# Optimization experiments

Hardware: AMD Instinct MI355X
Metric: run time of the kernel (lower is better)

The kernel has to match this reference:

```python
import jax, jax.numpy as jnp
import numpy as np

N_NODES = 50000   # nodes per channel
N_EDGES = 800000  # intra edges per channel (avg degree ~16)
N_GRAPHS = 64     # graphs in the batch (global_add_pool segments)
D = 128           # node_features_len == out_channels
L = 3             # n_layers
BN_EPS = 1e-5
NEG_SLOPE = 0.01  # F.leaky_relu default


def setup_inputs() -> dict:
    key = jax.random.key(0)
    ks = jax.random.split(key, 24)
    s = 0.05
    inp = {
        "x1": jax.random.normal(ks[0], (N_NODES, D), jnp.float32),
        "x2": jax.random.normal(ks[1], (N_NODES, D), jnp.float32),
        # GIN MLP channel 1: Linear-BN-ReLU-Linear-ReLU, stacked over layers
        "W1_ch1": jax.random.normal(ks[2], (L, D, D), jnp.float32) * s,
        "b1_ch1": jax.random.normal(ks[3], (L, D), jnp.float32) * s,
        "bn_g": 1.0 + jax.random.normal(ks[4], (L, D), jnp.float32) * s,
        "bn_b": jax.random.normal(ks[5], (L, D), jnp.float32) * s,
        "bn_m": jax.random.normal(ks[6], (L, D), jnp.float32) * s,
        "bn_v": 0.5 + jax.random.uniform(ks[7], (L, D), jnp.float32),
        "W2_ch1": jax.random.normal(ks[8], (L, D, D), jnp.float32) * s,
        "b2_ch1": jax.random.normal(ks[9], (L, D), jnp.float32) * s,
        # GIN MLP channel 2: Linear-ReLU-Linear
        "W1_ch2": jax.random.normal(ks[10], (L, D, D), jnp.float32) * s,
        "b1_ch2": jax.random.normal(ks[11], (L, D), jnp.float32) * s,
        "W2_ch2": jax.random.normal(ks[12], (L, D, D), jnp.float32) * s,
        "b2_ch2": jax.random.normal(ks[13], (L, D), jnp.float32) * s,
        # head: Linear(2*D*L -> D) - ReLU - Dropout - Linear(D -> 1)
        "Wf1": jax.random.normal(ks[14], (2 * D * L, D), jnp.float32) * s,
        "bf1": jax.random.normal(ks[15], (D,), jnp.float32) * s,
        "Wf2": jax.random.normal(ks[16], (D, 1), jnp.float32) * s,
        "bf2": jax.random.normal(ks[17], (1,), jnp.float32) * s,
        "edge1": jax.random.randint(ks[18], (2, N_EDGES), 0, N_NODES, dtype=jnp.int32),
        "edge2": jax.random.randint(ks[19], (2, N_EDGES), 0, N_NODES, dtype=jnp.int32),
        "batch1": jnp.sort(jax.random.randint(ks[20], (N_NODES,), 0, N_GRAPHS, dtype=jnp.int32)),
        "batch2": jnp.sort(jax.random.randint(ks[21], (N_NODES,), 0, N_GRAPHS, dtype=jnp.int32)),
    }
    return inp


def _aggregate(x, edge):
    # GINConv sum aggregation: message x[src] scattered to dst; eps=0 default
    return jax.ops.segment_sum(x[edge[0]], edge[1], num_segments=N_NODES)


def _channel1(x, edge, batch, W1, b1, g, b, m, v, W2, b2):
    pooled = []
    for i in range(L):
        h = (x + _aggregate(x, edge)) @ W1[i] + b1[i]
        h = (h - m[i]) * (g[i] / jnp.sqrt(v[i] + BN_EPS)) + b[i]  # eval-mode BN
        h = jax.nn.relu(h)
        h = jax.nn.relu(h @ W2[i] + b2[i])
        x = jax.nn.leaky_relu(h, NEG_SLOPE)
        pooled.append(jax.ops.segment_sum(x, batch, num_segments=N_GRAPHS))
    return jnp.concatenate(pooled, axis=-1)  # [G, D*L]


def _channel2(x, edge, batch, W1, b1, W2, b2):
    pooled = []
    for i in range(L):
        h = jax.nn.relu((x + _aggregate(x, edge)) @ W1[i] + b1[i])
        h = h @ W2[i] + b2[i]
        x = jax.nn.leaky_relu(h, NEG_SLOPE)
        pooled.append(jax.ops.segment_sum(x, batch, num_segments=N_GRAPHS))
    return jnp.concatenate(pooled, axis=-1)  # [G, D*L]


def reference(x1, x2, W1_ch1, b1_ch1, bn_g, bn_b, bn_m, bn_v, W2_ch1, b2_ch1,
              W1_ch2, b1_ch2, W2_ch2, b2_ch2, Wf1, bf1, Wf2, bf2,
              edge1, edge2, batch1, batch2):
    p1 = _channel1(x1, edge1, batch1, W1_ch1, b1_ch1, bn_g, bn_b, bn_m, bn_v, W2_ch1, b2_ch1)
    p2 = _channel2(x2, edge2, batch2, W1_ch2, b1_ch2, W2_ch2, b2_ch2)
    z = jnp.concatenate([p1, p2], axis=-1)  # [G, 2*D*L]
    h = jax.nn.relu(z @ Wf1 + bf1)          # dropout is identity in eval mode
    return h @ Wf2 + bf2                    # [G, 1]
```

## Files before the change

kernel.cpp:

```cpp
#include <hip/hip_runtime.h>

#define NN 50000
#define NE 800000
#define TOTN (2 * NN)
#define NG 64
#define DD 128
#define NL 3
#define ZW (2 * DD * NL)
#define NB2 128
#define NPB 391
#define CAP2 8192
#define CHUNK 4096
#define P1B 196
#define GB2 1024
#define AGGB (TOTN / 16)
#define CVTX (TOTN * DD / 8 / 256)

typedef __attribute__((ext_vector_type(8))) short short8;
typedef __attribute__((ext_vector_type(4))) float f32x4;

__device__ inline unsigned short f2bf(float f) {
  unsigned int u = __float_as_uint(f);
  unsigned int r = (u + 0x7fffu + ((u >> 16) & 1u)) >> 16;
  return (unsigned short)r;
}
__device__ inline float bflo(unsigned int u) { return __uint_as_float(u << 16); }
__device__ inline float bfhi(unsigned int u) { return __uint_as_float(u & 0xffff0000u); }

__global__ __launch_bounds__(256) void prep_kernel(
    const float* __restrict__ x1, const float* __restrict__ x2,
    unsigned short* __restrict__ X,
    const float* __restrict__ p0, const float* __restrict__ p1,
    const float* __restrict__ p2, const float* __restrict__ p3,
    unsigned short* __restrict__ WT,
    const int* __restrict__ e1, const int* __restrict__ e2,
    int* __restrict__ bcur, uint2* __restrict__ pairs) {
  int bid = blockIdx.x;
  if (bid < CVTX) {
    int i = bid * 256 + threadIdx.x;
    const int per = NN * DD / 8;
    int ch = i >= per;
    const float* x = ch ? x2 : x1;
    int il = i - ch * per;
    const float4* in4 = reinterpret_cast<const float4*>(x);
    float4 a = in4[2 * il], b = in4[2 * il + 1];
    uint4 o;
    o.x = (unsigned int)f2bf(a.x) | ((unsigned int)f2bf(a.y) << 16);
    o.y = (unsigned int)f2bf(a.z) | ((unsigned int)f2bf(a.w) << 16);
    o.z = (unsigned int)f2bf(b.x) | ((unsigned int)f2bf(b.y) << 16);
    o.w = (unsigned int)f2bf(b.z) | ((unsigned int)f2bf(b.w) << 16);
    reinterpret_cast<uint4*>(X)[i] = o;
    return;
  }
  if (bid < CVTX + 192) {
    __shared__ float tile[32][33];
    int idx = bid - CVTX;
    int k0 = (idx & 3) * 32, c0 = ((idx >> 2) & 3) * 32, slot = idx >> 4;
    int grp = slot / 3, mat = slot % 3;
    const float* ip = (grp == 0 ? p0 : grp == 1 ? p1 : grp == 2 ? p2 : p3) + mat * 16384;
    unsigned short* op = WT + slot * 16384;
    int tx = threadIdx.x & 31, ty = threadIdx.x >> 5;
#pragma unroll
    for (int rr = 0; rr < 32; rr += 8)
      tile[ty + rr][tx] = ip[(k0 + ty + rr) * 128 + (c0 + tx)];
    __syncthreads();
#pragma unroll
    for (int rr = 0; rr < 32; rr += 8)
      op[(c0 + ty + rr) * 128 + (k0 + tx)] = f2bf(tile[tx][ty + rr]);
    return;
  }
  {
    int blk = bid - (CVTX + 192);
    int ch = blk >= P1B;
    blk -= ch * P1B;
    const int* E = ch ? e2 : e1;
    int base = blk * CHUNK;
    __shared__ int lcnt[NB2], gbase[NB2];
    for (int i = threadIdx.x; i < NB2; i += 256) lcnt[i] = 0;
    __syncthreads();
    int srcv[16], dstv[16], lrank[16];
#pragma unroll
    for (int k = 0; k < 16; k++) {
      int e = base + k * 256 + threadIdx.x;
      if (e < NE) {
        srcv[k] = E[e];
        dstv[k] = E[NE + e];
        lrank[k] = atomicAdd(&lcnt[dstv[k] / NPB], 1);
      } else dstv[k] = -1;
    }
    __syncthreads();
    for (int i = threadIdx.x; i < NB2; i += 256)
      gbase[i] = atomicAdd(&bcur[ch * NB2 + i], lcnt[i]);
    __syncthreads();
#pragma unroll
    for (int k = 0; k < 16; k++)
      if (dstv[k] >= 0) {
        int g = dstv[k] / NPB;
        pairs[(size_t)(ch * NB2 + g) * CAP2 + gbase[g] + lrank[k]] =
            make_uint2((unsigned)srcv[k], (unsigned)dstv[k]);
      }
  }
}

__global__ __launch_bounds__(256) void scan_gstart_kernel(const int* __restrict__ bcur,
                                                          int* __restrict__ colbase,
                                                          const int* __restrict__ batch1,
                                                          const int* __restrict__ batch2,
                                                          int* __restrict__ gstart) {
  if (blockIdx.x == 0) {
    __shared__ int s[256];
    int tid = threadIdx.x;
    int v = bcur[tid];
    s[tid] = v;
    __syncthreads();
    int segstart = tid & ~127;
    for (int o = 1; o < 128; o <<= 1) {
      int t = (tid - o >= segstart) ? s[tid - o] : 0;
      __syncthreads();
      s[tid] += t;
      __syncthreads();
    }
    colbase[tid] = s[tid] - v;
  } else {
    int t = threadIdx.x;
    if (t >= 2 * (NG + 1)) return;
    int ch = t / (NG + 1), g = t % (NG + 1);
    const int* b = ch ? batch2 : batch1;
    int lo = 0, hi = NN;
    while (lo < hi) {
      int m = (lo + hi) >> 1;
      if (b[m] < g) lo = m + 1; else hi = m;
    }
    gstart[t] = lo;
  }
}

__global__ __launch_bounds__(256) void csr_build_kernel(const uint2* __restrict__ pairs,
                                                        const int* __restrict__ bcur,
                                                        const int* __restrict__ colbase,
                                                        int* __restrict__ rowptr,
                                                        int* __restrict__ col) {
  int g = blockIdx.x;
  int ch = g >> 7, b = g & 127;
  int node0 = b * NPB;
  int nloc = min(NPB, NN - node0);
  int count = bcur[g];
  int base = colbase[g];
  const uint2* p = pairs + (size_t)g * CAP2;
  __shared__ int hist[512], pref[512], cur[512], stmp[256];
  for (int i = threadIdx.x; i < 512; i += 256) hist[i] = 0;
  __syncthreads();
  for (int e = threadIdx.x; e < count; e += 256)
    atomicAdd(&hist[(int)p[e].y - node0], 1);
  __syncthreads();
  int t = threadIdx.x;
  int a0 = hist[2 * t], a1 = hist[2 * t + 1];
  int sum = a0 + a1;
  stmp[t] = sum;
  __syncthreads();
  for (int o = 1; o < 256; o <<= 1) {
    int tv = (t >= o) ? stmp[t - o] : 0;
    __syncthreads();
    stmp[t] += tv;
    __syncthreads();
  }
  int ex = stmp[t] - sum;
  pref[2 * t] = ex;       pref[2 * t + 1] = ex + a0;
  cur[2 * t] = ex;        cur[2 * t + 1] = ex + a0;
  __syncthreads();
  for (int i = threadIdx.x; i < nloc; i += 256)
    rowptr[ch * (NN + 1) + node0 + i] = base + pref[i];
  if (threadIdx.x == 0 && b == NB2 - 1) rowptr[ch * (NN + 1) + NN] = base + count;
  for (int e = threadIdx.x; e < count; e += 256) {
    uint2 pr = p[e];
    int pos = atomicAdd(&cur[(int)pr.y - node0], 1);
    col[ch * NE + base + pos] = (int)pr.x;
  }
}

__global__ __launch_bounds__(256) void agg_pool_kernel(const unsigned short* __restrict__ X,
                                                       const int* __restrict__ rowptr,
                                                       const int* __restrict__ col,
                                                       unsigned short* __restrict__ Y,
                                                       const unsigned short* __restrict__ Xprev,
                                                       const int* __restrict__ gstart,
                                                       float* __restrict__ z, int layerPrev) {
  if (blockIdx.x >= AGGB) {
    int pb = blockIdx.x - AGGB;
    int ch = pb >> 6, g = pb & 63;
    int r0 = gstart[ch * (NG + 1) + g], r1 = gstart[ch * (NG + 1) + g + 1];
    int c8 = threadIdx.x & 15, part = threadIdx.x >> 4;
    const uint4* X4 = reinterpret_cast<const uint4*>(Xprev);
    size_t base = (size_t)ch * NN * 16 + c8;
    float acc[8];
#pragma unroll
    for (int q = 0; q < 8; q++) acc[q] = 0.f;
    int r = r0 + part;
    for (; r + 48 < r1; r += 64) {
      uint4 v0 = X4[base + (size_t)r * 16];
      uint4 v1 = X4[base + (size_t)(r + 16) * 16];
      uint4 v2 = X4[base + (size_t)(r + 32) * 16];
      uint4 v3 = X4[base + (size_t)(r + 48) * 16];
      unsigned int w0[4] = {v0.x, v0.y, v0.z, v0.w};
      unsigned int w1[4] = {v1.x, v1.y, v1.z, v1.w};
      unsigned int w2[4] = {v2.x, v2.y, v2.z, v2.w};
      unsigned int w3[4] = {v3.x, v3.y, v3.z, v3.w};
#pragma unroll
      for (int q = 0; q < 4; q++) {
        acc[2 * q]     += bflo(w0[q]) + bflo(w1[q]) + bflo(w2[q]) + bflo(w3[q]);
        acc[2 * q + 1] += bfhi(w0[q]) + bfhi(w1[q]) + bfhi(w2[q]) + bfhi(w3[q]);
      }
    }
    for (; r < r1; r += 16) {
      uint4 v = X4[base + (size_t)r * 16];
      unsigned int w[4] = {v.x, v.y, v.z, v.w};
#pragma unroll
      for (int q = 0; q < 4; q++) {
        acc[2 * q]     += bflo(w[q]);
        acc[2 * q + 1] += bfhi(w[q]);
      }
    }
    __shared__ float zacc[16][128];
#pragma unroll
    for (int q = 0; q < 8; q++) zacc[part][c8 * 8 + q] = acc[q];
    __syncthreads();
    for (int s = 8; s > 0; s >>= 1) {
      if (part < s) {
#pragma unroll
        for (int q = 0; q < 8; q++)
          zacc[part][c8 * 8 + q] += zacc[part + s][c8 * 8 + q];
      }
      __syncthreads();
    }
    if (part == 0) {
#pragma unroll
      for (int q = 0; q < 8; q++) {
        int colw = c8 * 8 + q;
        z[(size_t)g * ZW + ch * DD * NL + layerPrev * DD + colw] = zacc[0][colw];
      }
    }
    return;
  }
  int node = blockIdx.x * 16 + (threadIdx.x >> 4);
  int lane = threadIdx.x & 15;
  int ch = node >= NN;
  int nl = node - ch * NN;
  const int* rp = rowptr + ch * (NN + 1);
  const int* cl = col + ch * NE;
  const uint4* X4 = reinterpret_cast<const uint4*>(X);
  size_t chbase = (size_t)ch * NN * 16;
  float acc[8];
  {
    uint4 sv = X4[(size_t)node * 16 + lane];
    unsigned int w[4] = {sv.x, sv.y, sv.z, sv.w};
#pragma unroll
    for (int q = 0; q < 4; q++) {
      acc[2 * q]     = bflo(w[q]);
      acc[2 * q + 1] = bfhi(w[q]);
    }
  }
  int s = rp[nl], e = rp[nl + 1];
  int j = s;
  for (; j + 8 <= e; j += 8) {
    uint4 v[8];
#pragma unroll
    for (int q = 0; q < 8; q++)
      v[q] = X4[chbase + (size_t)cl[j + q] * 16 + lane];
#pragma unroll
    for (int q = 0; q < 8; q++) {
      unsigned int w[4] = {v[q].x, v[q].y, v[q].z, v[q].w};
#pragma unroll
      for (int u = 0; u < 4; u++) {
        acc[2 * u]     += bflo(w[u]);
        acc[2 * u + 1] += bfhi(w[u]);
      }
    }
  }
  for (; j < e; ++j) {
    uint4 v = X4[chbase + (size_t)cl[j] * 16 + lane];
    unsigned int w[4] = {v.x, v.y, v.z, v.w};
#pragma unroll
    for (int u = 0; u < 4; u++) {
      acc[2 * u]     += bflo(w[u]);
      acc[2 * u + 1] += bfhi(w[u]);
    }
  }
  uint4 o;
  unsigned int* ow = reinterpret_cast<unsigned int*>(&o);
#pragma unroll
  for (int q = 0; q < 4; q++)
    ow[q] = (unsigned int)f2bf(acc[2 * q]) | ((unsigned int)f2bf(acc[2 * q + 1]) << 16);
  reinterpret_cast<uint4*>(Y)[(size_t)node * 16 + lane] = o;
}

__global__ __launch_bounds__(256) void gemm_fused_kernel(
    const unsigned short* __restrict__ Y, unsigned short* __restrict__ X,
    const unsigned short* __restrict__ WT,
    const float* __restrict__ b1c1, const float* __restrict__ b1c2,
    const float* __restrict__ b2c1, const float* __restrict__ b2c2,
    const float* __restrict__ bng, const float* __restrict__ bnb,
    const float* __restrict__ bnm, const float* __restrict__ bnv, int layer) {
  __shared__ unsigned short hlds[16][136];
  int ch = blockIdx.x >= GB2;
  int lane = threadIdx.x & 63, wv = threadIdx.x >> 6;
  int l15 = lane & 15, lk = lane >> 4;
  int c0 = wv * 32;
  const unsigned short* W1 = WT + (size_t)(ch * 6 + layer) * 16384;
  const unsigned short* W2 = WT + (size_t)(ch * 6 + 3 + layer) * 16384;
  short8 w1f[2][4], w2f[2][4];
#pragma unroll
  for (int ct = 0; ct < 2; ct++)
#pragma unroll
    for (int kk = 0; kk < 4; kk++) {
      size_t boff = (size_t)(c0 + ct * 16 + l15) * 128 + kk * 32 + lk * 8;
      w1f[ct][kk] = *reinterpret_cast<const short8*>(W1 + boff);
      w2f[ct][kk] = *reinterpret_cast<const short8*>(W2 + boff);
    }
  const float* b1 = (ch ? b1c2 : b1c1) + layer * DD;
  const float* b2 = (ch ? b2c2 : b2c1) + layer * DD;
  float sc1[2], sh1[2], sh2[2];
#pragma unroll
  for (int ct = 0; ct < 2; ct++) {
    int colg = c0 + ct * 16 + l15;
    if (!ch) {
      float s = bng[layer * DD + colg] * rsqrtf(bnv[layer * DD + colg] + 1e-5f);
      sc1[ct] = s;
      sh1[ct] = (b1[colg] - bnm[layer * DD + colg]) * s + bnb[layer * DD + colg];
    } else {
      sc1[ct] = 1.f;
      sh1[ct] = b1[colg];
    }
    sh2[ct] = b2[colg];
  }
  int t0 = ch ? blockIdx.x - GB2 : blockIdx.x;
  short8 a0, a1, a2, a3;
  {
    size_t r0g = (size_t)ch * NN + t0 * 16;
    const unsigned short* yp = Y + (r0g + l15) * 128 + lk * 8;
    a0 = *reinterpret_cast<const short8*>(yp);
    a1 = *reinterpret_cast<const short8*>(yp + 32);
    a2 = *reinterpret_cast<const short8*>(yp + 64);
    a3 = *reinterpret_cast<const short8*>(yp + 96);
  }
  for (int t = t0; t < 3125; t += GB2) {
    int r0l = t * 16;
    size_t r0g = (size_t)ch * NN + r0l;
    short8 n0, n1, n2, n3;
    int tn = t + GB2;
    if (tn < 3125) {
      const unsigned short* yp = Y + ((size_t)ch * NN + tn * 16 + l15) * 128 + lk * 8;
      n0 = *reinterpret_cast<const short8*>(yp);
      n1 = *reinterpret_cast<const short8*>(yp + 32);
      n2 = *reinterpret_cast<const short8*>(yp + 64);
      n3 = *reinterpret_cast<const short8*>(yp + 96);
    }
#pragma unroll
    for (int ct = 0; ct < 2; ct++) {
      f32x4 acc = {0.f, 0.f, 0.f, 0.f};
      acc = __builtin_amdgcn_mfma_f32_16x16x32_bf16(a0, w1f[ct][0], acc, 0, 0, 0);
      acc = __builtin_amdgcn_mfma_f32_16x16x32_bf16(a1, w1f[ct][1], acc, 0, 0, 0);
      acc = __builtin_amdgcn_mfma_f32_16x16x32_bf16(a2, w1f[ct][2], acc, 0, 0, 0);
      acc = __builtin_amdgcn_mfma_f32_16x16x32_bf16(a3, w1f[ct][3], acc, 0, 0, 0);
      int colg = c0 + ct * 16 + l15;
#pragma unroll
      for (int r = 0; r < 4; r++) {
        float tv = fmaxf(acc[r] * sc1[ct] + sh1[ct], 0.f);
        hlds[lk * 4 + r][colg] = f2bf(tv);
      }
    }
    __syncthreads();
    short8 h0 = *reinterpret_cast<const short8*>(&hlds[l15][lk * 8]);
    short8 h1 = *reinterpret_cast<const short8*>(&hlds[l15][32 + lk * 8]);
    short8 h2 = *reinterpret_cast<const short8*>(&hlds[l15][64 + lk * 8]);
    short8 h3 = *reinterpret_cast<const short8*>(&hlds[l15][96 + lk * 8]);
#pragma unroll
    for (int ct = 0; ct < 2; ct++) {
      f32x4 acc = {0.f, 0.f, 0.f, 0.f};
      acc = __builtin_amdgcn_mfma_f32_16x16x32_bf16(h0, w2f[ct][0], acc, 0, 0, 0);
      acc = __builtin_amdgcn_mfma_f32_16x16x32_bf16(h1, w2f[ct][1], acc, 0, 0, 0);
      acc = __builtin_amdgcn_mfma_f32_16x16x32_bf16(h2, w2f[ct][2], acc, 0, 0, 0);
      acc = __builtin_amdgcn_mfma_f32_16x16x32_bf16(h3, w2f[ct][3], acc, 0, 0, 0);
      int colg = c0 + ct * 16 + l15;
#pragma unroll
      for (int r = 0; r < 4; r++) {
        float tv = acc[r] + sh2[ct];
        if (!ch) tv = fmaxf(tv, 0.f);
        else     tv = tv > 0.f ? tv : 0.01f * tv;
        X[(r0g + lk * 4 + r) * 128 + colg] = f2bf(tv);
      }
    }
    __syncthreads();
    a0 = n0; a1 = n1; a2 = n2; a3 = n3;
  }
}

__global__ __launch_bounds__(256) void pool_kernel(const unsigned short* __restrict__ X,
                                                   const int* __restrict__ gstart,
                                                   float* __restrict__ z, int layer) {
  int ch = blockIdx.x >> 6, g = blockIdx.x & 63;
  int r0 = gstart[ch * (NG + 1) + g], r1 = gstart[ch * (NG + 1) + g + 1];
  int c8 = threadIdx.x & 15, part = threadIdx.x >> 4;
  const uint4* X4 = reinterpret_cast<const uint4*>(X);
  size_t base = (size_t)ch * NN * 16 + c8;
  float acc[8];
#pragma unroll
  for (int q = 0; q < 8; q++) acc[q] = 0.f;
  int r = r0 + part;
  for (; r + 48 < r1; r += 64) {
    uint4 v0 = X4[base + (size_t)r * 16];
    uint4 v1 = X4[base + (size_t)(r + 16) * 16];
    uint4 v2 = X4[base + (size_t)(r + 32) * 16];
    uint4 v3 = X4[base + (size_t)(r + 48) * 16];
    unsigned int w0[4] = {v0.x, v0.y, v0.z, v0.w};
    unsigned int w1[4] = {v1.x, v1.y, v1.z, v1.w};
    unsigned int w2[4] = {v2.x, v2.y, v2.z, v2.w};
    unsigned int w3[4] = {v3.x, v3.y, v3.z, v3.w};
#pragma unroll
    for (int q = 0; q < 4; q++) {
      acc[2 * q]     += bflo(w0[q]) + bflo(w1[q]) + bflo(w2[q]) + bflo(w3[q]);
      acc[2 * q + 1] += bfhi(w0[q]) + bfhi(w1[q]) + bfhi(w2[q]) + bfhi(w3[q]);
    }
  }
  for (; r < r1; r += 16) {
    uint4 v = X4[base + (size_t)r * 16];
    unsigned int w[4] = {v.x, v.y, v.z, v.w};
#pragma unroll
    for (int q = 0; q < 4; q++) {
      acc[2 * q]     += bflo(w[q]);
      acc[2 * q + 1] += bfhi(w[q]);
    }
  }
  __shared__ float zacc[16][128];
#pragma unroll
  for (int q = 0; q < 8; q++) zacc[part][c8 * 8 + q] = acc[q];
  __syncthreads();
  for (int s = 8; s > 0; s >>= 1) {
    if (part < s) {
#pragma unroll
      for (int q = 0; q < 8; q++)
        zacc[part][c8 * 8 + q] += zacc[part + s][c8 * 8 + q];
    }
    __syncthreads();
  }
  if (part == 0) {
#pragma unroll
    for (int q = 0; q < 8; q++) {
      int colw = c8 * 8 + q;
      z[(size_t)g * ZW + ch * DD * NL + layer * DD + colw] = zacc[0][colw];
    }
  }
}

__global__ __launch_bounds__(128) void head_kernel(const float* __restrict__ z,
                                                   const float* __restrict__ Wf1,
                                                   const float* __restrict__ bf1,
                                                   const float* __restrict__ Wf2,
                                                   const float* __restrict__ bf2,
                                                   float* __restrict__ out) {
  int g = blockIdx.x, t = threadIdx.x;
  const float* zr = z + (size_t)g * ZW;
  float acc = bf1[t];
  for (int j = 0; j < ZW; ++j) acc += zr[j] * Wf1[(size_t)j * DD + t];
  float h = fmaxf(acc, 0.f);
  __shared__ float red[128];
  red[t] = h * Wf2[t];
  __syncthreads();
  for (int s = 64; s > 0; s >>= 1) {
    if (t < s) red[t] += red[t + s];
    __syncthreads();
  }
  if (t == 0) out[g] = red[0] + bf2[0];
}

extern "C" void kernel_launch(void* const* d_in, const int* in_sizes, int n_in,
                              void* d_out, int out_size, void* d_ws, size_t ws_size,
                              hipStream_t stream) {
  const float* x1   = (const float*)d_in[0];
  const float* x2   = (const float*)d_in[1];
  const float* W1c1 = (const float*)d_in[2];
  const float* b1c1 = (const float*)d_in[3];
  const float* bng  = (const float*)d_in[4];
  const float* bnb  = (const float*)d_in[5];
  const float* bnm  = (const float*)d_in[6];
  const float* bnv  = (const float*)d_in[7];
  const float* W2c1 = (const float*)d_in[8];
  const float* b2c1 = (const float*)d_in[9];
  const float* W1c2 = (const float*)d_in[10];
  const float* b1c2 = (const float*)d_in[11];
  const float* W2c2 = (const float*)d_in[12];
  const float* b2c2 = (const float*)d_in[13];
  const float* Wf1  = (const float*)d_in[14];
  const float* bf1  = (const float*)d_in[15];
  const float* Wf2  = (const float*)d_in[16];
  const float* bf2  = (const float*)d_in[17];
  const int* edge1  = (const int*)d_in[18];
  const int* edge2  = (const int*)d_in[19];
  const int* batch1 = (const int*)d_in[20];
  const int* batch2 = (const int*)d_in[21];
  (void)ws_size; (void)n_in; (void)in_sizes; (void)out_size;

  char* ws = (char*)d_ws;
  const size_t NB16 = (size_t)TOTN * DD * 2;
  unsigned short* bufA = (unsigned short*)(ws);
  unsigned short* bufB = (unsigned short*)(ws + NB16);
  unsigned short* bufY = (unsigned short*)(ws + 2 * NB16);
  size_t off = 3 * NB16;
  unsigned short* WT = (unsigned short*)(ws + off); off += (size_t)12 * 16384 * 2;
  uint2* pairs = (uint2*)(ws + off); off += (size_t)2 * NB2 * CAP2 * 8;
  int* col     = (int*)(ws + off); off += (size_t)2 * NE * 4;
  int* rowptr  = (int*)(ws + off); off += (((size_t)2 * (NN + 1) * 4) + 255) & ~(size_t)255;
  int* bcur    = (int*)(ws + off); off += 256 * 4;
  int* colbase = (int*)(ws + off); off += 256 * 4;
  int* gstart  = (int*)(ws + off); off += 256 * 4;
  float* z     = (float*)(ws + off); off += (size_t)NG * ZW * 4;

  hipMemsetAsync(bcur, 0, 256 * 4, stream);
  prep_kernel<<<CVTX + 192 + 2 * P1B, 256, 0, stream>>>(
      x1, x2, bufA, W1c1, W2c1, W1c2, W2c2, WT, edge1, edge2, bcur, pairs);
  scan_gstart_kernel<<<2, 256, 0, stream>>>(bcur, colbase, batch1, batch2, gstart);
  csr_build_kernel<<<2 * NB2, 256, 0, stream>>>(pairs, bcur, colbase, rowptr, col);

  unsigned short* cin = bufA;
  unsigned short* cout = bufB;
  for (int i = 0; i < NL; ++i) {
    int grid = (i == 0) ? AGGB : AGGB + 2 * NG;
    agg_pool_kernel<<<grid, 256, 0, stream>>>(cin, rowptr, col, bufY,
                                              cin, gstart, z, i - 1);
    gemm_fused_kernel<<<2 * GB2, 256, 0, stream>>>(bufY, cout, WT,
                                                   b1c1, b1c2, b2c1, b2c2,
                                                   bng, bnb, bnm, bnv, i);
    unsigned short* tmp = cin; cin = cout; cout = tmp;
  }
  pool_kernel<<<2 * NG, 256, 0, stream>>>(cin, gstart, z, NL - 1);
  head_kernel<<<NG, 128, 0, stream>>>(z, Wf1, bf1, Wf2, bf2, (float*)d_out);
}
```

Baseline: 375.9 us.

## Interleave channel aggregation with other channel's GEMM in phased kernel launches

```diff
diff --git a/kernel.cpp b/kernel.cpp
--- a/kernel.cpp
+++ b/kernel.cpp
@@ -2,7 +2,6 @@
 
 #define NN 50000
 #define NE 800000
-#define TOTN (2 * NN)
 #define NG 64
 #define DD 128
 #define NL 3
@@ -12,9 +11,9 @@
 #define CAP2 8192
 #define CHUNK 4096
 #define P1B 196
-#define GB2 1024
-#define AGGB (TOTN / 16)
-#define CVTX (TOTN * DD / 8 / 256)
+#define TILES 3125
+#define GEMMB 1024
+#define CVTX 6250
 
 typedef __attribute__((ext_vector_type(8))) short short8;
 typedef __attribute__((ext_vector_type(4))) float f32x4;
@@ -29,7 +28,7 @@
 
 __global__ __launch_bounds__(256) void prep_kernel(
     const float* __restrict__ x1, const float* __restrict__ x2,
-    unsigned short* __restrict__ X,
+    unsigned short* __restrict__ X0, unsigned short* __restrict__ X1,
     const float* __restrict__ p0, const float* __restrict__ p1,
     const float* __restrict__ p2, const float* __restrict__ p3,
     unsigned short* __restrict__ WT,
@@ -41,6 +40,7 @@
     const int per = NN * DD / 8;
     int ch = i >= per;
     const float* x = ch ? x2 : x1;
+    unsigned short* X = ch ? X1 : X0;
     int il = i - ch * per;
     const float4* in4 = reinterpret_cast<const float4*>(x);
     float4 a = in4[2 * il], b = in4[2 * il + 1];
@@ -49,7 +49,7 @@
     o.y = (unsigned int)f2bf(a.z) | ((unsigned int)f2bf(a.w) << 16);
     o.z = (unsigned int)f2bf(b.x) | ((unsigned int)f2bf(b.y) << 16);
     o.w = (unsigned int)f2bf(b.z) | ((unsigned int)f2bf(b.w) << 16);
-    reinterpret_cast<uint4*>(X)[i] = o;
+    reinterpret_cast<uint4*>(X)[il] = o;
     return;
   }
   if (bid < CVTX + 192) {
@@ -102,26 +102,14 @@
   }
 }
 
-__global__ __launch_bounds__(256) void scan_gstart_kernel(const int* __restrict__ bcur,
-                                                          int* __restrict__ colbase,
-                                                          const int* __restrict__ batch1,
-                                                          const int* __restrict__ batch2,
-                                                          int* __restrict__ gstart) {
-  if (blockIdx.x == 0) {
-    __shared__ int s[256];
-    int tid = threadIdx.x;
-    int v = bcur[tid];
-    s[tid] = v;
-    __syncthreads();
-    int segstart = tid & ~127;
-    for (int o = 1; o < 128; o <<= 1) {
-      int t = (tid - o >= segstart) ? s[tid - o] : 0;
-      __syncthreads();
-      s[tid] += t;
-      __syncthreads();
-    }
-    colbase[tid] = s[tid] - v;
-  } else {
+__global__ __launch_bounds__(256) void csr_build_kernel(const uint2* __restrict__ pairs,
+                                                        const int* __restrict__ bcur,
+                                                        int* __restrict__ rowptr,
+                                                        int* __restrict__ col,
+                                                        const int* __restrict__ batch1,
+                                                        const int* __restrict__ batch2,
+                                                        int* __restrict__ gstart) {
+  if (blockIdx.x == 256) {
     int t = threadIdx.x;
     if (t >= 2 * (NG + 1)) return;
     int ch = t / (NG + 1), g = t % (NG + 1);
@@ -132,75 +120,233 @@
       if (b[m] < g) lo = m + 1; else hi = m;
     }
     gstart[t] = lo;
-  }
-}
-
-__global__ __launch_bounds__(256) void csr_build_kernel(const uint2* __restrict__ pairs,
-                                                        const int* __restrict__ bcur,
-                                                        const int* __restrict__ colbase,
-                                                        int* __restrict__ rowptr,
-                                                        int* __restrict__ col) {
+    return;
+  }
   int g = blockIdx.x;
   int ch = g >> 7, b = g & 127;
+  int tid = threadIdx.x;
+  __shared__ int sc[128];
+  if (tid < 128) sc[tid] = bcur[ch * 128 + tid];
+  __syncthreads();
+  for (int o = 1; o < 128; o <<= 1) {
+    int t = (tid < 128 && tid >= o) ? sc[tid - o] : 0;
+    __syncthreads();
+    if (tid < 128) sc[tid] += t;
+    __syncthreads();
+  }
+  int count = bcur[g];
+  int base = sc[b] - count;
   int node0 = b * NPB;
   int nloc = min(NPB, NN - node0);
-  int count = bcur[g];
-  int base = colbase[g];
   const uint2* p = pairs + (size_t)g * CAP2;
   __shared__ int hist[512], pref[512], cur[512], stmp[256];
-  for (int i = threadIdx.x; i < 512; i += 256) hist[i] = 0;
-  __syncthreads();
-  for (int e = threadIdx.x; e < count; e += 256)
+  for (int i = tid; i < 512; i += 256) hist[i] = 0;
+  __syncthreads();
+  for (int e = tid; e < count; e += 256)
     atomicAdd(&hist[(int)p[e].y - node0], 1);
   __syncthreads();
-  int t = threadIdx.x;
-  int a0 = hist[2 * t], a1 = hist[2 * t + 1];
+  int a0 = hist[2 * tid], a1 = hist[2 * tid + 1];
   int sum = a0 + a1;
-  stmp[t] = sum;
+  stmp[tid] = sum;
   __syncthreads();
   for (int o = 1; o < 256; o <<= 1) {
-    int tv = (t >= o) ? stmp[t - o] : 0;
-    __syncthreads();
-    stmp[t] += tv;
-    __syncthreads();
-  }
-  int ex = stmp[t] - sum;
-  pref[2 * t] = ex;       pref[2 * t + 1] = ex + a0;
-  cur[2 * t] = ex;        cur[2 * t + 1] = ex + a0;
-  __syncthreads();
-  for (int i = threadIdx.x; i < nloc; i += 256)
+    int tv = (tid >= o) ? stmp[tid - o] : 0;
+    __syncthreads();
+    stmp[tid] += tv;
+    __syncthreads();
+  }
+  int ex = stmp[tid] - sum;
+  pref[2 * tid] = ex;       pref[2 * tid + 1] = ex + a0;
+  cur[2 * tid] = ex;        cur[2 * tid + 1] = ex + a0;
+  __syncthreads();
+  for (int i = tid; i < nloc; i += 256)
     rowptr[ch * (NN + 1) + node0 + i] = base + pref[i];
-  if (threadIdx.x == 0 && b == NB2 - 1) rowptr[ch * (NN + 1) + NN] = base + count;
-  for (int e = threadIdx.x; e < count; e += 256) {
+  if (tid == 0 && b == NB2 - 1) rowptr[ch * (NN + 1) + NN] = base + count;
+  for (int e = tid; e < count; e += 256) {
     uint2 pr = p[e];
     int pos = atomicAdd(&cur[(int)pr.y - node0], 1);
     col[ch * NE + base + pos] = (int)pr.x;
   }
 }
 
-__global__ __launch_bounds__(256) void agg_pool_kernel(const unsigned short* __restrict__ X,
-                                                       const int* __restrict__ rowptr,
-                                                       const int* __restrict__ col,
-                                                       unsigned short* __restrict__ Y,
-                                                       const unsigned short* __restrict__ Xprev,
-                                                       const int* __restrict__ gstart,
-                                                       float* __restrict__ z, int layerPrev) {
-  if (blockIdx.x >= AGGB) {
-    int pb = blockIdx.x - AGGB;
-    int ch = pb >> 6, g = pb & 63;
+__global__ __launch_bounds__(256) void phase_kernel(
+    int doAgg, const unsigned short* __restrict__ aggIn,
+    unsigned short* __restrict__ aggOut, int aggCh,
+    const int* __restrict__ rowptr, const int* __restrict__ col,
+    int doGemm, const unsigned short* __restrict__ gemmIn,
+    unsigned short* __restrict__ gemmOut, int gemmCh, int gemmLayer,
+    const unsigned short* __restrict__ WT,
+    const float* __restrict__ b1c1, const float* __restrict__ b1c2,
+    const float* __restrict__ b2c1, const float* __restrict__ b2c2,
+    const float* __restrict__ bng, const float* __restrict__ bnb,
+    const float* __restrict__ bnm, const float* __restrict__ bnv,
+    const unsigned short* __restrict__ poolIn, int poolCh, int poolLayer,
+    const int* __restrict__ gstart, float* __restrict__ z) {
+  __shared__ __align__(16) char smem[8192];
+  int bid = blockIdx.x;
+  int role, idx;
+  if (doAgg) {
+    if (doGemm) {
+      if (bid < 4096) {
+        if ((bid & 3) == 3) { role = 1; idx = bid >> 2; }
+        else                { role = 0; idx = (bid >> 2) * 3 + (bid & 3); }
+      } else if (bid < 4096 + 53) { role = 0; idx = 3072 + (bid - 4096); }
+      else { role = 2; idx = bid - (4096 + 53); }
+    } else {
+      if (bid < TILES) { role = 0; idx = bid; }
+      else             { role = 2; idx = bid - TILES; }
+    }
+  } else if (doGemm) {
+    if (bid < GEMMB) { role = 1; idx = bid; }
+    else             { role = 2; idx = bid - GEMMB; }
+  } else { role = 2; idx = bid; }
+
+  if (role == 0) {
+    int node = idx * 16 + (threadIdx.x >> 4);
+    int lane = threadIdx.x & 15;
+    const int* rp = rowptr + aggCh * (NN + 1);
+    const int* cl = col + aggCh * NE;
+    const uint4* X4 = reinterpret_cast<const uint4*>(aggIn);
+    float acc[8];
+    {
+      uint4 sv = X4[(size_t)node * 16 + lane];
+      unsigned int w[4] = {sv.x, sv.y, sv.z, sv.w};
+#pragma unroll
+      for (int q = 0; q < 4; q++) {
+        acc[2 * q]     = bflo(w[q]);
+        acc[2 * q + 1] = bfhi(w[q]);
+      }
+    }
+    int s = rp[node], e = rp[node + 1];
+    int j = s;
+    for (; j + 8 <= e; j += 8) {
+      uint4 v[8];
+#pragma unroll
+      for (int q = 0; q < 8; q++)
+        v[q] = X4[(size_t)cl[j + q] * 16 + lane];
+#pragma unroll
+      for (int q = 0; q < 8; q++) {
+        unsigned int w[4] = {v[q].x, v[q].y, v[q].z, v[q].w};
+#pragma unroll
+        for (int u = 0; u < 4; u++) {
+          acc[2 * u]     += bflo(w[u]);
+          acc[2 * u + 1] += bfhi(w[u]);
+        }
+      }
+    }
+    for (; j < e; ++j) {
+      uint4 v = X4[(size_t)cl[j] * 16 + lane];
+      unsigned int w[4] = {v.x, v.y, v.z, v.w};
+#pragma unroll
+      for (int u = 0; u < 4; u++) {
+        acc[2 * u]     += bflo(w[u]);
+        acc[2 * u + 1] += bfhi(w[u]);
+      }
+    }
+    uint4 o;
+    unsigned int* ow = reinterpret_cast<unsigned int*>(&o);
+#pragma unroll
+    for (int q = 0; q < 4; q++)
+      ow[q] = (unsigned int)f2bf(acc[2 * q]) | ((unsigned int)f2bf(acc[2 * q + 1]) << 16);
+    reinterpret_cast<uint4*>(aggOut)[(size_t)node * 16 + lane] = o;
+    return;
+  }
+
+  if (role == 1) {
+    unsigned short (*hlds)[136] = reinterpret_cast<unsigned short (*)[136]>(smem);
+    int ch = gemmCh;
+    int lane = threadIdx.x & 63, wv = threadIdx.x >> 6;
+    int l15 = lane & 15, lk = lane >> 4;
+    int c0 = wv * 32;
+    const unsigned short* W1 = WT + (size_t)(ch * 6 + gemmLayer) * 16384;
+    const unsigned short* W2 = WT + (size_t)(ch * 6 + 3 + gemmLayer) * 16384;
+    short8 w1f[2][4], w2f[2][4];
+#pragma unroll
+    for (int ct = 0; ct < 2; ct++)
+#pragma unroll
+      for (int kk = 0; kk < 4; kk++) {
+        size_t boff = (size_t)(c0 + ct * 16 + l15) * 128 + kk * 32 + lk * 8;
+        w1f[ct][kk] = *reinterpret_cast<const short8*>(W1 + boff);
+        w2f[ct][kk] = *reinterpret_cast<const short8*>(W2 + boff);
+      }
+    const float* b1 = (ch ? b1c2 : b1c1) + gemmLayer * DD;
+    const float* b2 = (ch ? b2c2 : b2c1) + gemmLayer * DD;
+    float sc1[2], sh1[2], sh2[2];
+#pragma unroll
+    for (int ct = 0; ct < 2; ct++) {
+      int colg = c0 + ct * 16 + l15;
+      if (!ch) {
+        float s = bng[gemmLayer * DD + colg] * rsqrtf(bnv[gemmLayer * DD + colg] + 1e-5f);
+        sc1[ct] = s;
+        sh1[ct] = (b1[colg] - bnm[gemmLayer * DD + colg]) * s + bnb[gemmLayer * DD + colg];
+      } else {
+        sc1[ct] = 1.f;
+        sh1[ct] = b1[colg];
+      }
+      sh2[ct] = b2[colg];
+    }
+    for (int t = idx; t < TILES; t += GEMMB) {
+      size_t r0 = (size_t)t * 16;
+      const unsigned short* yp = gemmIn + (r0 + l15) * 128 + lk * 8;
+      short8 a0 = *reinterpret_cast<const short8*>(yp);
+      short8 a1 = *reinterpret_cast<const short8*>(yp + 32);
+      short8 a2 = *reinterpret_cast<const short8*>(yp + 64);
+      short8 a3 = *reinterpret_cast<const short8*>(yp + 96);
+#pragma unroll
+      for (int ct = 0; ct < 2; ct++) {
+        f32x4 acc = {0.f, 0.f, 0.f, 0.f};
+        acc = __builtin_amdgcn_mfma_f32_16x16x32_bf16(a0, w1f[ct][0], acc, 0, 0, 0);
+        acc = __builtin_amdgcn_mfma_f32_16x16x32_bf16(a1, w1f[ct][1], acc, 0, 0, 0);
+        acc = __builtin_amdgcn_mfma_f32_16x16x32_bf16(a2, w1f[ct][2], acc, 0, 0, 0);
+        acc = __builtin_amdgcn_mfma_f32_16x16x32_bf16(a3, w1f[ct][3], acc, 0, 0, 0);
+        int colg = c0 + ct * 16 + l15;
+#pragma unroll
+        for (int r = 0; r < 4; r++) {
+          float tv = fmaxf(acc[r] * sc1[ct] + sh1[ct], 0.f);
+          hlds[lk * 4 + r][colg] = f2bf(tv);
+        }
+      }
+      __syncthreads();
+      short8 h0 = *reinterpret_cast<const short8*>(&hlds[l15][lk * 8]);
+      short8 h1 = *reinterpret_cast<const short8*>(&hlds[l15][32 + lk * 8]);
+      short8 h2 = *reinterpret_cast<const short8*>(&hlds[l15][64 + lk * 8]);
+      short8 h3 = *reinterpret_cast<const short8*>(&hlds[l15][96 + lk * 8]);
+#pragma unroll
+      for (int ct = 0; ct < 2; ct++) {
+        f32x4 acc = {0.f, 0.f, 0.f, 0.f};
+        acc = __builtin_amdgcn_mfma_f32_16x16x32_bf16(h0, w2f[ct][0], acc, 0, 0, 0);
+        acc = __builtin_amdgcn_mfma_f32_16x16x32_bf16(h1, w2f[ct][1], acc, 0, 0, 0);
+        acc = __builtin_amdgcn_mfma_f32_16x16x32_bf16(h2, w2f[ct][2], acc, 0, 0, 0);
+        acc = __builtin_amdgcn_mfma_f32_16x16x32_bf16(h3, w2f[ct][3], acc, 0, 0, 0);
+        int colg = c0 + ct * 16 + l15;
+#pragma unroll
+        for (int r = 0; r < 4; r++) {
+          float tv = acc[r] + sh2[ct];
+          if (!ch) tv = fmaxf(tv, 0.f);
+          else     tv = tv > 0.f ? tv : 0.01f * tv;
+          gemmOut[(r0 + lk * 4 + r) * 128 + colg] = f2bf(tv);
+        }
+      }
+      __syncthreads();
+    }
+    return;
+  }
+
+  {
+    float (*zacc)[128] = reinterpret_cast<float (*)[128]>(smem);
+    int ch = poolCh, g = idx;
     int r0 = gstart[ch * (NG + 1) + g], r1 = gstart[ch * (NG + 1) + g + 1];
     int c8 = threadIdx.x & 15, part = threadIdx.x >> 4;
-    const uint4* X4 = reinterpret_cast<const uint4*>(Xprev);
-    size_t base = (size_t)ch * NN * 16 + c8;
+    const uint4* X4 = reinterpret_cast<const uint4*>(poolIn);
     float acc[8];
 #pragma unroll
     for (int q = 0; q < 8; q++) acc[q] = 0.f;
     int r = r0 + part;
     for (; r + 48 < r1; r += 64) {
-      uint4 v0 = X4[base + (size_t)r * 16];
-      uint4 v1 = X4[base + (size_t)(r + 16) * 16];
-      uint4 v2 = X4[base + (size_t)(r + 32) * 16];
-      uint4 v3 = X4[base + (size_t)(r + 48) * 16];
+      uint4 v0 = X4[(size_t)r * 16 + c8];
+      uint4 v1 = X4[(size_t)(r + 16) * 16 + c8];
+      uint4 v2 = X4[(size_t)(r + 32) * 16 + c8];
+      uint4 v3 = X4[(size_t)(r + 48) * 16 + c8];
       unsigned int w0[4] = {v0.x, v0.y, v0.z, v0.w};
       unsigned int w1[4] = {v1.x, v1.y, v1.z, v1.w};
       unsigned int w2[4] = {v2.x, v2.y, v2.z, v2.w};
@@ -212,7 +358,7 @@
       }
     }
     for (; r < r1; r += 16) {
-      uint4 v = X4[base + (size_t)r * 16];
+      uint4 v = X4[(size_t)r * 16 + c8];
       unsigned int w[4] = {v.x, v.y, v.z, v.w};
 #pragma unroll
       for (int q = 0; q < 4; q++) {
@@ -220,7 +366,6 @@
         acc[2 * q + 1] += bfhi(w[q]);
       }
     }
-    __shared__ float zacc[16][128];
 #pragma unroll
     for (int q = 0; q < 8; q++) zacc[part][c8 * 8 + q] = acc[q];
     __syncthreads();
@@ -236,217 +381,8 @@
 #pragma unroll
       for (int q = 0; q < 8; q++) {
         int colw = c8 * 8 + q;
-        z[(size_t)g * ZW + ch * DD * NL + layerPrev * DD + colw] = zacc[0][colw];
-      }
-    }
-    return;
-  }
-  int node = blockIdx.x * 16 + (threadIdx.x >> 4);
-  int lane = threadIdx.x & 15;
-  int ch = node >= NN;
-  int nl = node - ch * NN;
-  const int* rp = rowptr + ch * (NN + 1);
-  const int* cl = col + ch * NE;
-  const uint4* X4 = reinterpret_cast<const uint4*>(X);
-  size_t chbase = (size_t)ch * NN * 16;
-  float acc[8];
-  {
-    uint4 sv = X4[(size_t)node * 16 + lane];
-    unsigned int w[4] = {sv.x, sv.y, sv.z, sv.w};
-#pragma unroll
-    for (int q = 0; q < 4; q++) {
-      acc[2 * q]     = bflo(w[q]);
-      acc[2 * q + 1] = bfhi(w[q]);
-    }
-  }
-  int s = rp[nl], e = rp[nl + 1];
-  int j = s;
-  for (; j + 8 <= e; j += 8) {
-    uint4 v[8];
-#pragma unroll
-    for (int q = 0; q < 8; q++)
-      v[q] = X4[chbase + (size_t)cl[j + q] * 16 + lane];
-#pragma unroll
-    for (int q = 0; q < 8; q++) {
-      unsigned int w[4] = {v[q].x, v[q].y, v[q].z, v[q].w};
-#pragma unroll
-      for (int u = 0; u < 4; u++) {
-        acc[2 * u]     += bflo(w[u]);
-        acc[2 * u + 1] += bfhi(w[u]);
-      }
-    }
-  }
-  for (; j < e; ++j) {
-    uint4 v = X4[chbase + (size_t)cl[j] * 16 + lane];
-    unsigned int w[4] = {v.x, v.y, v.z, v.w};
-#pragma unroll
-    for (int u = 0; u < 4; u++) {
-      acc[2 * u]     += bflo(w[u]);
-      acc[2 * u + 1] += bfhi(w[u]);
-    }
-  }
-  uint4 o;
-  unsigned int* ow = reinterpret_cast<unsigned int*>(&o);
-#pragma unroll
-  for (int q = 0; q < 4; q++)
-    ow[q] = (unsigned int)f2bf(acc[2 * q]) | ((unsigned int)f2bf(acc[2 * q + 1]) << 16);
-  reinterpret_cast<uint4*>(Y)[(size_t)node * 16 + lane] = o;
-}
-
-__global__ __launch_bounds__(256) void gemm_fused_kernel(
-    const unsigned short* __restrict__ Y, unsigned short* __restrict__ X,
-    const unsigned short* __restrict__ WT,
-    const float* __restrict__ b1c1, const float* __restrict__ b1c2,
-    const float* __restrict__ b2c1, const float* __restrict__ b2c2,
-    const float* __restrict__ bng, const float* __restrict__ bnb,
-    const float* __restrict__ bnm, const float* __restrict__ bnv, int layer) {
-  __shared__ unsigned short hlds[16][136];
-  int ch = blockIdx.x >= GB2;
-  int lane = threadIdx.x & 63, wv = threadIdx.x >> 6;
-  int l15 = lane & 15, lk = lane >> 4;
-  int c0 = wv * 32;
-  const unsigned short* W1 = WT + (size_t)(ch * 6 + layer) * 16384;
-  const unsigned short* W2 = WT + (size_t)(ch * 6 + 3 + layer) * 16384;
-  short8 w1f[2][4], w2f[2][4];
-#pragma unroll
-  for (int ct = 0; ct < 2; ct++)
-#pragma unroll
-    for (int kk = 0; kk < 4; kk++) {
-      size_t boff = (size_t)(c0 + ct * 16 + l15) * 128 + kk * 32 + lk * 8;
-      w1f[ct][kk] = *reinterpret_cast<const short8*>(W1 + boff);
-      w2f[ct][kk] = *reinterpret_cast<const short8*>(W2 + boff);
-    }
-  const float* b1 = (ch ? b1c2 : b1c1) + layer * DD;
-  const float* b2 = (ch ? b2c2 : b2c1) + layer * DD;
-  float sc1[2], sh1[2], sh2[2];
-#pragma unroll
-  for (int ct = 0; ct < 2; ct++) {
-    int colg = c0 + ct * 16 + l15;
-    if (!ch) {
-      float s = bng[layer * DD + colg] * rsqrtf(bnv[layer * DD + colg] + 1e-5f);
-      sc1[ct] = s;
-      sh1[ct] = (b1[colg] - bnm[layer * DD + colg]) * s + bnb[layer * DD + colg];
-    } else {
-      sc1[ct] = 1.f;
-      sh1[ct] = b1[colg];
-    }
-    sh2[ct] = b2[colg];
-  }
-  int t0 = ch ? blockIdx.x - GB2 : blockIdx.x;
-  short8 a0, a1, a2, a3;
-  {
-    size_t r0g = (size_t)ch * NN + t0 * 16;
-    const unsigned short* yp = Y + (r0g + l15) * 128 + lk * 8;
-    a0 = *reinterpret_cast<const short8*>(yp);
-    a1 = *reinterpret_cast<const short8*>(yp + 32);
-    a2 = *reinterpret_cast<const short8*>(yp + 64);
-    a3 = *reinterpret_cast<const short8*>(yp + 96);
-  }
-  for (int t = t0; t < 3125; t += GB2) {
-    int r0l = t * 16;
-    size_t r0g = (size_t)ch * NN + r0l;
-    short8 n0, n1, n2, n3;
-    int tn = t + GB2;
-    if (tn < 3125) {
-      const unsigned short* yp = Y + ((size_t)ch * NN + tn * 16 + l15) * 128 + lk * 8;
-      n0 = *reinterpret_cast<const short8*>(yp);
-      n1 = *reinterpret_cast<const short8*>(yp + 32);
-      n2 = *reinterpret_cast<const short8*>(yp + 64);
-      n3 = *reinterpret_cast<const short8*>(yp + 96);
-    }
-#pragma unroll
-    for (int ct = 0; ct < 2; ct++) {
-      f32x4 acc = {0.f, 0.f, 0.f, 0.f};
-      acc = __builtin_amdgcn_mfma_f32_16x16x32_bf16(a0, w1f[ct][0], acc, 0, 0, 0);
-      acc = __builtin_amdgcn_mfma_f32_16x16x32_bf16(a1, w1f[ct][1], acc, 0, 0, 0);
-      acc = __builtin_amdgcn_mfma_f32_16x16x32_bf16(a2, w1f[ct][2], acc, 0, 0, 0);
-      acc = __builtin_amdgcn_mfma_f32_16x16x32_bf16(a3, w1f[ct][3], acc, 0, 0, 0);
-      int colg = c0 + ct * 16 + l15;
-#pragma unroll
-      for (int r = 0; r < 4; r++) {
-        float tv = fmaxf(acc[r] * sc1[ct] + sh1[ct], 0.f);
-        hlds[lk * 4 + r][colg] = f2bf(tv);
-      }
-    }
-    __syncthreads();
-    short8 h0 = *reinterpret_cast<const short8*>(&hlds[l15][lk * 8]);
-    short8 h1 = *reinterpret_cast<const short8*>(&hlds[l15][32 + lk * 8]);
-    short8 h2 = *reinterpret_cast<const short8*>(&hlds[l15][64 + lk * 8]);
-    short8 h3 = *reinterpret_cast<const short8*>(&hlds[l15][96 + lk * 8]);
-#pragma unroll
-    for (int ct = 0; ct < 2; ct++) {
-      f32x4 acc = {0.f, 0.f, 0.f, 0.f};
-      acc = __builtin_amdgcn_mfma_f32_16x16x32_bf16(h0, w2f[ct][0], acc, 0, 0, 0);
-      acc = __builtin_amdgcn_mfma_f32_16x16x32_bf16(h1, w2f[ct][1], acc, 0, 0, 0);
-      acc = __builtin_amdgcn_mfma_f32_16x16x32_bf16(h2, w2f[ct][2], acc, 0, 0, 0);
-      acc = __builtin_amdgcn_mfma_f32_16x16x32_bf16(h3, w2f[ct][3], acc, 0, 0, 0);
-      int colg = c0 + ct * 16 + l15;
-#pragma unroll
-      for (int r = 0; r < 4; r++) {
-        float tv = acc[r] + sh2[ct];
-        if (!ch) tv = fmaxf(tv, 0.f);
-        else     tv = tv > 0.f ? tv : 0.01f * tv;
-        X[(r0g + lk * 4 + r) * 128 + colg] = f2bf(tv);
-      }
-    }
-    __syncthreads();
-    a0 = n0; a1 = n1; a2 = n2; a3 = n3;
-  }
-}
-
-__global__ __launch_bounds__(256) void pool_kernel(const unsigned short* __restrict__ X,
-                                                   const int* __restrict__ gstart,
-                                                   float* __restrict__ z, int layer) {
-  int ch = blockIdx.x >> 6, g = blockIdx.x & 63;
-  int r0 = gstart[ch * (NG + 1) + g], r1 = gstart[ch * (NG + 1) + g + 1];
-  int c8 = threadIdx.x & 15, part = threadIdx.x >> 4;
-  const uint4* X4 = reinterpret_cast<const uint4*>(X);
-  size_t base = (size_t)ch * NN * 16 + c8;
-  float acc[8];
-#pragma unroll
-  for (int q = 0; q < 8; q++) acc[q] = 0.f;
-  int r = r0 + part;
-  for (; r + 48 < r1; r += 64) {
-    uint4 v0 = X4[base + (size_t)r * 16];
-    uint4 v1 = X4[base + (size_t)(r + 16) * 16];
-    uint4 v2 = X4[base + (size_t)(r + 32) * 16];
-    uint4 v3 = X4[base + (size_t)(r + 48) * 16];
-    unsigned int w0[4] = {v0.x, v0.y, v0.z, v0.w};
-    unsigned int w1[4] = {v1.x, v1.y, v1.z, v1.w};
-    unsigned int w2[4] = {v2.x, v2.y, v2.z, v2.w};
-    unsigned int w3[4] = {v3.x, v3.y, v3.z, v3.w};
-#pragma unroll
-    for (int q = 0; q < 4; q++) {
-      acc[2 * q]     += bflo(w0[q]) + bflo(w1[q]) + bflo(w2[q]) + bflo(w3[q]);
-      acc[2 * q + 1] += bfhi(w0[q]) + bfhi(w1[q]) + bfhi(w2[q]) + bfhi(w3[q]);
-    }
-  }
-  for (; r < r1; r += 16) {
-    uint4 v = X4[base + (size_t)r * 16];
-    unsigned int w[4] = {v.x, v.y, v.z, v.w};
-#pragma unroll
-    for (int q = 0; q < 4; q++) {
-      acc[2 * q]     += bflo(w[q]);
-      acc[2 * q + 1] += bfhi(w[q]);
-    }
-  }
-  __shared__ float zacc[16][128];
-#pragma unroll
-  for (int q = 0; q < 8; q++) zacc[part][c8 * 8 + q] = acc[q];
-  __syncthreads();
-  for (int s = 8; s > 0; s >>= 1) {
-    if (part < s) {
-#pragma unroll
-      for (int q = 0; q < 8; q++)
-        zacc[part][c8 * 8 + q] += zacc[part + s][c8 * 8 + q];
-    }
-    __syncthreads();
-  }
-  if (part == 0) {
-#pragma unroll
-    for (int q = 0; q < 8; q++) {
-      int colw = c8 * 8 + q;
-      z[(size_t)g * ZW + ch * DD * NL + layer * DD + colw] = zacc[0][colw];
+        z[(size_t)g * ZW + ch * DD * NL + poolLayer * DD + colw] = zacc[0][colw];
+      }
     }
   }
 }
@@ -500,37 +436,45 @@
   (void)ws_size; (void)n_in; (void)in_sizes; (void)out_size;
 
   char* ws = (char*)d_ws;
-  const size_t NB16 = (size_t)TOTN * DD * 2;
-  unsigned short* bufA = (unsigned short*)(ws);
-  unsigned short* bufB = (unsigned short*)(ws + NB16);
-  unsigned short* bufY = (unsigned short*)(ws + 2 * NB16);
-  size_t off = 3 * NB16;
+  const size_t CB = (size_t)NN * DD * 2;
+  unsigned short* A0 = (unsigned short*)(ws);
+  unsigned short* B0 = (unsigned short*)(ws + CB);
+  unsigned short* Y0 = (unsigned short*)(ws + 2 * CB);
+  unsigned short* A1 = (unsigned short*)(ws + 3 * CB);
+  unsigned short* B1 = (unsigned short*)(ws + 4 * CB);
+  unsigned short* Y1 = (unsigned short*)(ws + 5 * CB);
+  size_t off = 6 * CB;
   unsigned short* WT = (unsigned short*)(ws + off); off += (size_t)12 * 16384 * 2;
   uint2* pairs = (uint2*)(ws + off); off += (size_t)2 * NB2 * CAP2 * 8;
   int* col     = (int*)(ws + off); off += (size_t)2 * NE * 4;
   int* rowptr  = (int*)(ws + off); off += (((size_t)2 * (NN + 1) * 4) + 255) & ~(size_t)255;
   int* bcur    = (int*)(ws + off); off += 256 * 4;
-  int* colbase = (int*)(ws + off); off += 256 * 4;
   int* gstart  = (int*)(ws + off); off += 256 * 4;
   float* z     = (float*)(ws + off); off += (size_t)NG * ZW * 4;
 
   hipMemsetAsync(bcur, 0, 256 * 4, stream);
   prep_kernel<<<CVTX + 192 + 2 * P1B, 256, 0, stream>>>(
-      x1, x2, bufA, W1c1, W2c1, W1c2, W2c2, WT, edge1, edge2, bcur, pairs);
-  scan_gstart_kernel<<<2, 256, 0, stream>>>(bcur, colbase, batch1, batch2, gstart);
-  csr_build_kernel<<<2 * NB2, 256, 0, stream>>>(pairs, bcur, colbase, rowptr, col);
-
-  unsigned short* cin = bufA;
-  unsigned short* cout = bufB;
-  for (int i = 0; i < NL; ++i) {
-    int grid = (i == 0) ? AGGB : AGGB + 2 * NG;
-    agg_pool_kernel<<<grid, 256, 0, stream>>>(cin, rowptr, col, bufY,
-                                              cin, gstart, z, i - 1);
-    gemm_fused_kernel<<<2 * GB2, 256, 0, stream>>>(bufY, cout, WT,
-                                                   b1c1, b1c2, b2c1, b2c2,
-                                                   bng, bnb, bnm, bnv, i);
-    unsigned short* tmp = cin; cin = cout; cout = tmp;
-  }
-  pool_kernel<<<2 * NG, 256, 0, stream>>>(cin, gstart, z, NL - 1);
+      x1, x2, A0, A1, W1c1, W2c1, W1c2, W2c2, WT, edge1, edge2, bcur, pairs);
+  csr_build_kernel<<<257, 256, 0, stream>>>(pairs, bcur, rowptr, col, batch1, batch2, gstart);
+
+#define PHASE(grid, dA, aIn, aOut, aCh, dG, gIn, gOut, gCh, gL, pIn, pCh, pL)           \
+  phase_kernel<<<grid, 256, 0, stream>>>(dA, aIn, aOut, aCh, rowptr, col,               \
+                                         dG, gIn, gOut, gCh, gL, WT,                    \
+                                         b1c1, b1c2, b2c1, b2c2, bng, bnb, bnm, bnv,    \
+                                         pIn, pCh, pL, gstart, z)
+
+  const int GA  = TILES;
+  const int GAG = 4096 + 53;
+  const int GAGP = GAG + 2 * NG / 2;
+  PHASE(GA,  1, A0, Y0, 0,  0, (unsigned short*)0, (unsigned short*)0, 0, 0,  (unsigned short*)0, 0, 0);
+  PHASE(GAG, 1, A1, Y1, 1,  1, Y0, B0, 0, 0,  (unsigned short*)0, 0, 0);
+  PHASE(GAGP, 1, B0, Y0, 0,  1, Y1, B1, 1, 0,  B0, 0, 0);
+  PHASE(GAGP, 1, B1, Y1, 1,  1, Y0, A0, 0, 1,  B1, 1, 0);
+  PHASE(GAGP, 1, A0, Y0, 0,  1, Y1, A1, 1, 1,  A0, 0, 1);
+  PHASE(GAGP, 1, A1, Y1, 1,  1, Y0, B0, 0, 2,  A1, 1, 1);
+  PHASE(GEMMB + 2 * NG / 2, 0, (unsigned short*)0, (unsigned short*)0, 0,  1, Y1, B1, 1, 2,  B0, 0, 2);
+  PHASE(2 * NG / 2, 0, (unsigned short*)0, (unsigned short*)0, 0,  0, (unsigned short*)0, (unsigned short*)0, 0, 0,  B1, 1, 2);
+#undef PHASE
+
   head_kernel<<<NG, 128, 0, stream>>>(z, Wf1, bf1, Wf2, bf2, (float*)d_out);
 }
```

Result: slower. 454.3 us (+20.8%).
